# Kernel tuning notes

Hardware: AMD Instinct MI355X
Metric: run time of the kernel (lower is better)

Reference implementation:

```python
import jax, jax.numpy as jnp
import numpy as np

B, T, D = 32, 512, 768
DUR_MAX = 8.0


def length_regulate(x, dur):
    # dur[dur < 0] = 0; reps = (dur + 0.5).long()  (floor of dur+0.5 for dur >= 0)
    dur = jnp.maximum(dur, 0.0)
    reps = jnp.floor(dur + 0.5).astype(jnp.int32)          # [B, T]
    cum = jnp.cumsum(reps, axis=1)                          # [B, T] end offsets
    totals = cum[:, -1]                                     # [B] per-sample lengths
    t_out = int(jnp.max(totals))                            # padded output length (data-dependent, eager)
    pos = jnp.arange(t_out, dtype=jnp.int32)                # [Tout]
    # For output slot j, source token index = searchsorted(cum, j, 'right')
    idx = jax.vmap(lambda c: jnp.searchsorted(c, pos, side='right'))(cum)  # [B, Tout]
    idx = jnp.minimum(idx, x.shape[1] - 1)                  # clamp padding region
    out = jnp.take_along_axis(x, idx[..., None], axis=1)    # [B, Tout, D] gather
    mask = pos[None, :] < totals[:, None]                   # [B, Tout]
    return jnp.where(mask[..., None], out, jnp.zeros((), x.dtype))


def setup_inputs() -> dict:
    key = jax.random.key(0)
    k1, k2 = jax.random.split(key)
    x = jax.random.normal(k1, (B, T, D), dtype=jnp.float32)
    dur = jax.random.uniform(k2, (B, T), dtype=jnp.float32, minval=0.0, maxval=DUR_MAX)
    return {"x": x, "dur": dur}


def reference(x, dur):
    return length_regulate(x, dur)
```

## Files before the change

kernel.cpp:

```cpp
#include <hip/hip_runtime.h>

#define BB 32
#define TT 512
#define DD 768
#define NTHREADS 192
#define TOK_PER_BLOCK 8
#define BLOCKS_PER_BATCH (TT / TOK_PER_BLOCK)

typedef float f4 __attribute__((ext_vector_type(4)));

__global__ __launch_bounds__(NTHREADS) void lr_fused_kernel(
    const float* __restrict__ x, const float* __restrict__ dur,
    float* __restrict__ out, int t_out) {
    __shared__ int scum[TT];
    const int b = blockIdx.y;
    const int tid = threadIdx.x;

    for (int i = tid; i < TT; i += NTHREADS) {
        float d = fmaxf(dur[b * TT + i], 0.0f);
        scum[i] = (int)floorf(d + 0.5f);
    }
    __syncthreads();

    #pragma unroll
    for (int off = 1; off < TT; off <<= 1) {
        const int i0 = tid, i1 = tid + NTHREADS, i2 = tid + 2 * NTHREADS;
        int v0 = (i0 >= off) ? scum[i0 - off] : 0;
        int v1 = (i1 >= off) ? scum[i1 - off] : 0;
        int v2 = (i2 < TT && i2 >= off) ? scum[i2 - off] : 0;
        __syncthreads();
        scum[i0] += v0;
        scum[i1] += v1;
        if (i2 < TT) scum[i2] += v2;
        __syncthreads();
    }

    const int s0 = blockIdx.x * TOK_PER_BLOCK;
    const f4* xb = (const f4*)(x + (size_t)b * TT * DD);
    f4* ob = (f4*)(out + (size_t)b * (size_t)t_out * DD);

    #pragma unroll
    for (int k = 0; k < TOK_PER_BLOCK; ++k) {
        const int t = s0 + k;
        const int start = (t == 0) ? 0 : scum[t - 1];
        const int end = scum[t];
        if (end > start) {
            const f4 v = xb[(size_t)t * NTHREADS + tid];
            for (int p = start; p < end; ++p)
                __builtin_nontemporal_store(v, &ob[(size_t)p * NTHREADS + tid]);
        }
    }

    const int total = scum[TT - 1];
    const f4 z = (f4)(0.0f);
    for (int pos = total + blockIdx.x; pos < t_out; pos += BLOCKS_PER_BATCH)
        __builtin_nontemporal_store(z, &ob[(size_t)pos * NTHREADS + tid]);
}

extern "C" void kernel_launch(void* const* d_in, const int* in_sizes, int n_in,
                              void* d_out, int out_size, void* d_ws, size_t ws_size,
                              hipStream_t stream) {
    const float* x   = (const float*)d_in[0];
    const float* dur = (const float*)d_in[1];
    float* out = (float*)d_out;
    (void)d_ws; (void)ws_size;

    const int t_out = out_size / (BB * DD);

    dim3 grid(BLOCKS_PER_BATCH, BB);
    lr_fused_kernel<<<grid, NTHREADS, 0, stream>>>(x, dur, out, t_out);
}
```

Measured before the change: 252.7 us.

## Partition work by output rows instead of source tokens for load balance

Each block now owns a contiguous range of output rows rather than a fixed set of source tokens. It locates the first source token by binary search over the shared prefix sum, then walks forward, prefetching the next token's vector while storing the current one, and zero-fills the rows past the sample's total. This evens out per-block store work, which the token-based split left dependent on duration values. The cost is a binary search per block and a sequential scan over tokens.

```diff
diff --git a/kernel.cpp b/kernel.cpp
--- a/kernel.cpp
+++ b/kernel.cpp
@@ -4,17 +4,20 @@
 #define TT 512
 #define DD 768
 #define NTHREADS 192
-#define TOK_PER_BLOCK 8
-#define BLOCKS_PER_BATCH (TT / TOK_PER_BLOCK)
+#define BLOCKS_PER_BATCH 64
 
 typedef float f4 __attribute__((ext_vector_type(4)));
 
-__global__ __launch_bounds__(NTHREADS) void lr_fused_kernel(
+__global__ __launch_bounds__(NTHREADS) void lr_balanced_kernel(
     const float* __restrict__ x, const float* __restrict__ dur,
-    float* __restrict__ out, int t_out) {
+    float* __restrict__ out, int t_out, int rpb) {
     __shared__ int scum[TT];
     const int b = blockIdx.y;
     const int tid = threadIdx.x;
+
+    const int r0 = blockIdx.x * rpb;
+    const int r1 = (r0 + rpb < t_out) ? (r0 + rpb) : t_out;
+    if (r0 >= r1) return;
 
     for (int i = tid; i < TT; i += NTHREADS) {
         float d = fmaxf(dur[b * TT + i], 0.0f);
@@ -35,26 +38,44 @@
         __syncthreads();
     }
 
-    const int s0 = blockIdx.x * TOK_PER_BLOCK;
+    const int total = scum[TT - 1];
     const f4* xb = (const f4*)(x + (size_t)b * TT * DD);
-    f4* ob = (f4*)(out + (size_t)b * (size_t)t_out * DD);
+    f4* ob = (f4*)(out + (size_t)b * (size_t)t_out * DD) + tid;
 
-    #pragma unroll
-    for (int k = 0; k < TOK_PER_BLOCK; ++k) {
-        const int t = s0 + k;
-        const int start = (t == 0) ? 0 : scum[t - 1];
-        const int end = scum[t];
-        if (end > start) {
-            const f4 v = xb[(size_t)t * NTHREADS + tid];
-            for (int p = start; p < end; ++p)
-                __builtin_nontemporal_store(v, &ob[(size_t)p * NTHREADS + tid]);
+    const int rcopy = (r1 < total) ? r1 : total;
+    int r = r0;
+
+    if (r < rcopy) {
+        int lo = 0, hi = TT;
+        while (lo < hi) {
+            int mid = (lo + hi) >> 1;
+            if (scum[mid] <= r) lo = mid + 1; else hi = mid;
+        }
+        int t = lo;
+
+        f4 v = xb[(size_t)t * NTHREADS + tid];
+        f4* op = ob + (size_t)r * NTHREADS;
+        for (;;) {
+            int stop = scum[t];
+            if (stop >= rcopy) {
+                for (; r < rcopy; ++r, op += NTHREADS)
+                    __builtin_nontemporal_store(v, op);
+                break;
+            }
+            int tn = t + 1;
+            while (scum[tn] <= stop) ++tn;
+            const f4 vn = xb[(size_t)tn * NTHREADS + tid];
+            for (; r < stop; ++r, op += NTHREADS)
+                __builtin_nontemporal_store(v, op);
+            v = vn; t = tn;
         }
     }
 
-    const int total = scum[TT - 1];
+    const int z0 = (r0 > total) ? r0 : total;
     const f4 z = (f4)(0.0f);
-    for (int pos = total + blockIdx.x; pos < t_out; pos += BLOCKS_PER_BATCH)
-        __builtin_nontemporal_store(z, &ob[(size_t)pos * NTHREADS + tid]);
+    f4* opz = ob + (size_t)z0 * NTHREADS;
+    for (int rz = z0; rz < r1; ++rz, opz += NTHREADS)
+        __builtin_nontemporal_store(z, opz);
 }
 
 extern "C" void kernel_launch(void* const* d_in, const int* in_sizes, int n_in,
@@ -63,10 +84,11 @@
     const float* x   = (const float*)d_in[0];
     const float* dur = (const float*)d_in[1];
     float* out = (float*)d_out;
-    (void)d_ws; (void)ws_size;
+    (void)d_ws; (void)ws_size; (void)in_sizes; (void)n_in;
 
     const int t_out = out_size / (BB * DD);
+    const int rpb = (t_out + BLOCKS_PER_BATCH - 1) / BLOCKS_PER_BATCH;
 
     dim3 grid(BLOCKS_PER_BATCH, BB);
-    lr_fused_kernel<<<grid, NTHREADS, 0, stream>>>(x, dur, out, t_out);
+    lr_balanced_kernel<<<grid, NTHREADS, 0, stream>>>(x, dur, out, t_out, rpb);
 }
```

Result: no change. 256.7 us (+1.6%).

## Split into scan+searchsorted kernel and per-output-row gather kernel

Applied to the files above, without the earlier changes.

Replaces the fused kernel, where each block scanned durations and then scattered its tokens with nontemporal stores, with two kernels. The first computes the prefix sum and, by binary search, a source index for every output row, written to workspace. The second gathers one output row per block with regular stores. This evens out the load imbalance from variable repeat counts, at the cost of an extra launch, an index round trip through global memory, and losing the nontemporal stores.

```diff
diff --git a/kernel.cpp b/kernel.cpp
--- a/kernel.cpp
+++ b/kernel.cpp
@@ -3,58 +3,56 @@
 #define BB 32
 #define TT 512
 #define DD 768
-#define NTHREADS 192
-#define TOK_PER_BLOCK 8
-#define BLOCKS_PER_BATCH (TT / TOK_PER_BLOCK)
+#define NLANES 192
 
 typedef float f4 __attribute__((ext_vector_type(4)));
 
-__global__ __launch_bounds__(NTHREADS) void lr_fused_kernel(
-    const float* __restrict__ x, const float* __restrict__ dur,
-    float* __restrict__ out, int t_out) {
+
+__global__ __launch_bounds__(TT) void lr_scan_kernel(
+    const float* __restrict__ dur, int* __restrict__ idx, int t_out) {
     __shared__ int scum[TT];
-    const int b = blockIdx.y;
+    const int b = blockIdx.x;
     const int tid = threadIdx.x;
 
-    for (int i = tid; i < TT; i += NTHREADS) {
-        float d = fmaxf(dur[b * TT + i], 0.0f);
-        scum[i] = (int)floorf(d + 0.5f);
-    }
+    float d = fmaxf(dur[b * TT + tid], 0.0f);
+    scum[tid] = (int)floorf(d + 0.5f);
     __syncthreads();
 
     #pragma unroll
     for (int off = 1; off < TT; off <<= 1) {
-        const int i0 = tid, i1 = tid + NTHREADS, i2 = tid + 2 * NTHREADS;
-        int v0 = (i0 >= off) ? scum[i0 - off] : 0;
-        int v1 = (i1 >= off) ? scum[i1 - off] : 0;
-        int v2 = (i2 < TT && i2 >= off) ? scum[i2 - off] : 0;
+        int v = (tid >= off) ? scum[tid - off] : 0;
         __syncthreads();
-        scum[i0] += v0;
-        scum[i1] += v1;
-        if (i2 < TT) scum[i2] += v2;
+        scum[tid] += v;
         __syncthreads();
     }
 
-    const int s0 = blockIdx.x * TOK_PER_BLOCK;
-    const f4* xb = (const f4*)(x + (size_t)b * TT * DD);
-    f4* ob = (f4*)(out + (size_t)b * (size_t)t_out * DD);
+    const int total = scum[TT - 1];
+    for (int p = tid; p < t_out; p += TT) {
+        int v = -1;
+        if (p < total) {
+            int lo = 0, hi = TT;
+            while (lo < hi) {
+                int mid = (lo + hi) >> 1;
+                if (scum[mid] <= p) lo = mid + 1; else hi = mid;
+            }
+            v = lo;
+        }
+        idx[b * t_out + p] = v;
+    }
+}
 
-    #pragma unroll
-    for (int k = 0; k < TOK_PER_BLOCK; ++k) {
-        const int t = s0 + k;
-        const int start = (t == 0) ? 0 : scum[t - 1];
-        const int end = scum[t];
-        if (end > start) {
-            const f4 v = xb[(size_t)t * NTHREADS + tid];
-            for (int p = start; p < end; ++p)
-                __builtin_nontemporal_store(v, &ob[(size_t)p * NTHREADS + tid]);
-        }
-    }
+__global__ __launch_bounds__(NLANES) void lr_scatter_kernel(
+    const float* __restrict__ x, const int* __restrict__ idx,
+    float* __restrict__ out, int t_out) {
+    const int b = blockIdx.y;
+    const int r = blockIdx.x;
+    const int tid = threadIdx.x;
 
-    const int total = scum[TT - 1];
-    const f4 z = (f4)(0.0f);
-    for (int pos = total + blockIdx.x; pos < t_out; pos += BLOCKS_PER_BATCH)
-        __builtin_nontemporal_store(z, &ob[(size_t)pos * NTHREADS + tid]);
+    const int t = idx[b * t_out + r];
+    f4 v = (f4)(0.0f);
+    if (t >= 0)
+        v = ((const f4*)(x + (size_t)b * TT * DD))[(size_t)t * NLANES + tid];
+    ((f4*)(out + (size_t)b * (size_t)t_out * DD))[(size_t)r * NLANES + tid] = v;
 }
 
 extern "C" void kernel_launch(void* const* d_in, const int* in_sizes, int n_in,
@@ -63,10 +61,11 @@
     const float* x   = (const float*)d_in[0];
     const float* dur = (const float*)d_in[1];
     float* out = (float*)d_out;
-    (void)d_ws; (void)ws_size;
+    (void)in_sizes; (void)n_in; (void)ws_size;
 
     const int t_out = out_size / (BB * DD);
+    int* idx = (int*)d_ws;
 
-    dim3 grid(BLOCKS_PER_BATCH, BB);
-    lr_fused_kernel<<<grid, NTHREADS, 0, stream>>>(x, dur, out, t_out);
+    lr_scan_kernel<<<BB, TT, 0, stream>>>(dur, idx, t_out);
+    lr_scatter_kernel<<<dim3(t_out, BB), NLANES, 0, stream>>>(x, idx, out, t_out);
 }
```

Result: slower. 271.8 us (+7.6%).
